# Kernel optimization log

Measured on AMD Instinct MI355X. Metric: run time of the kernel, lower is better.

Reference implementation:

```python
import jax, jax.numpy as jnp
import numpy as np

N, E, D, L, G = 50000, 640000, 128, 5, 128
BN_EPS = 1e-5

def _bn(x, g, b):
    # training-mode batchnorm over axis 0, biased variance (torch semantics)
    m = x.mean(axis=0)
    v = x.var(axis=0)
    return (x - m) * jax.lax.rsqrt(v + BN_EPS) * g + b

def setup_inputs():
    key = jax.random.key(0)
    ks = iter(jax.random.split(key, 40))
    rn = lambda shape, s=0.05: jax.random.normal(next(ks), shape, jnp.float32) * s
    inp = {}
    inp['x'] = jax.random.randint(next(ks), (N, 1), 0, 300)
    inp['edge_index'] = jax.random.randint(next(ks), (2, E), 0, N)
    inp['edge_attr'] = jax.random.normal(next(ks), (E, 7), jnp.float32)
    inp['batch'] = jnp.sort(jax.random.randint(next(ks), (N,), 0, G))
    inp['node_emb'] = rn((300, D))
    inp['vn_emb'] = jnp.zeros((1, D), jnp.float32)
    inp['eps'] = jnp.zeros((L,), jnp.float32)
    inp['edge_W'] = rn((L, 7, D)); inp['edge_b'] = rn((L, D))
    inp['W1'] = rn((L, D, 2 * D)); inp['b1'] = rn((L, 2 * D))
    inp['bn1_g'] = 1.0 + rn((L, 2 * D)); inp['bn1_b'] = rn((L, 2 * D))
    inp['W2'] = rn((L, 2 * D, D)); inp['b2'] = rn((L, D))
    inp['bn_g'] = 1.0 + rn((L, D)); inp['bn_b'] = rn((L, D))
    inp['vn_W1'] = rn((L - 1, D, 2 * D)); inp['vn_b1'] = rn((L - 1, 2 * D))
    inp['vn_bn1_g'] = 1.0 + rn((L - 1, 2 * D)); inp['vn_bn1_b'] = rn((L - 1, 2 * D))
    inp['vn_W2'] = rn((L - 1, 2 * D, D)); inp['vn_b2'] = rn((L - 1, D))
    inp['vn_bn2_g'] = 1.0 + rn((L - 1, D)); inp['vn_bn2_b'] = rn((L - 1, D))
    return inp

def reference(x, edge_index, edge_attr, batch, node_emb, vn_emb, eps,
              edge_W, edge_b, W1, b1, bn1_g, bn1_b, W2, b2, bn_g, bn_b,
              vn_W1, vn_b1, vn_bn1_g, vn_bn1_b, vn_W2, vn_b2, vn_bn2_g, vn_bn2_b):
    src, dst = edge_index[0], edge_index[1]
    h = node_emb[x[:, 0]]                      # [N, D]
    vn = jnp.broadcast_to(vn_emb, (G, D))      # virtualnode state per graph
    for l in range(L):
        h_in = h + vn[batch]                   # virtualnode broadcast
        e = edge_attr @ edge_W[l] + edge_b[l]  # [E, D]
        msg = jax.nn.relu(h_in[src] + e)       # gather + fused elementwise
        agg = jax.ops.segment_sum(msg, dst, num_segments=N)
        z = (1.0 + eps[l]) * h_in + agg
        z = jax.nn.relu(_bn(z @ W1[l] + b1[l], bn1_g[l], bn1_b[l]))
        z = _bn(z @ W2[l] + b2[l], bn_g[l], bn_b[l])
        h_out = jax.nn.relu(z) if l != L - 1 else z
        if l < L - 1:
            pooled = jax.ops.segment_sum(h_in, batch, num_segments=G)
            v = vn + pooled
            v = jax.nn.relu(_bn(v @ vn_W1[l] + vn_b1[l], vn_bn1_g[l], vn_bn1_b[l]))
            vn = jax.nn.relu(_bn(v @ vn_W2[l] + vn_b2[l], vn_bn2_g[l], vn_bn2_b[l]))
        h = h_out
    return h
```

## Files before the change

kernel.cpp:

```cpp
#include <hip/hip_runtime.h>
#include <stdint.h>

#define NN 50000
#define EE 640000
#define DD 128
#define LL 5
#define GG 128
#define D2 256

using bf16x8 = __attribute__((ext_vector_type(8))) short;
using f32x4v = __attribute__((ext_vector_type(4))) float;
using u32x4v = __attribute__((ext_vector_type(4))) unsigned int;

__device__ __forceinline__ unsigned short f2bf(float f){
  union { float f; uint32_t u; } c; c.f = f;
  uint32_t u = c.u;
  uint32_t r = (u + 0x7FFFu + ((u >> 16) & 1u)) >> 16;
  return (unsigned short)r;
}
__device__ __forceinline__ float bf2f(unsigned short u){
  union { uint32_t u; float f; } c; c.u = ((uint32_t)u) << 16; return c.f;
}


__global__ __launch_bounds__(256) void zero_kernel(float* p, int n){
  int i = blockIdx.x*256 + threadIdx.x;
  if (i < n) p[i] = 0.f;
}

__global__ __launch_bounds__(256) void count_kernel(const int* __restrict__ ei, int* __restrict__ counts){
  int e = blockIdx.x*256 + threadIdx.x;
  if (e < EE) atomicAdd(&counts[ei[EE + e]], 1);
}

#define SCAN_B 512
__global__ __launch_bounds__(SCAN_B) void scan1_kernel(const int* __restrict__ counts, int* __restrict__ bsums, int n){
  __shared__ int sh[SCAN_B];
  int b = blockIdx.x, t = threadIdx.x;
  int i = b*SCAN_B + t;
  sh[t] = (i < n) ? counts[i] : 0;
  __syncthreads();
  for (int s = SCAN_B/2; s > 0; s >>= 1){
    if (t < s) sh[t] += sh[t+s];
    __syncthreads();
  }
  if (t == 0) bsums[b] = sh[0];
}

__global__ void scan2_kernel(int* bsums, int nb){
  if (threadIdx.x == 0){
    int run = 0;
    for (int i = 0; i < nb; ++i){ int v = bsums[i]; bsums[i] = run; run += v; }
  }
}

__global__ __launch_bounds__(SCAN_B) void scan3_kernel(const int* __restrict__ counts, const int* __restrict__ bsums,
                                                       int* __restrict__ startp, int* __restrict__ cursor, int n){
  __shared__ int sh[SCAN_B];
  int b = blockIdx.x, t = threadIdx.x;
  int i = b*SCAN_B + t;
  int v = (i < n) ? counts[i] : 0;
  sh[t] = v;
  __syncthreads();
  for (int s = 1; s < SCAN_B; s <<= 1){
    int add = (t >= s) ? sh[t-s] : 0;
    __syncthreads();
    sh[t] += add;
    __syncthreads();
  }
  int excl = sh[t] - v + bsums[b];
  if (i < n){ startp[i] = excl; cursor[i] = excl; }
  if (i == n-1) startp[n] = excl + v;
}

__global__ __launch_bounds__(256) void fill_kernel(const int* __restrict__ ei, int* __restrict__ cursor, int* __restrict__ csr){
  int e = blockIdx.x*256 + threadIdx.x;
  if (e < EE){
    int d = ei[EE + e];
    int slot = atomicAdd(&cursor[d], 1);
    csr[slot] = e;
  }
}

__global__ __launch_bounds__(256) void egather_kernel(const int* __restrict__ csr, const int* __restrict__ ei,
                                                      const float* __restrict__ ea,
                                                      int* __restrict__ csr_src, float* __restrict__ csr_ea8){
  int s = blockIdx.x*256 + threadIdx.x;
  if (s < EE){
    int e = csr[s];
    csr_src[s] = ei[e];
    float v[8];
    #pragma unroll
    for (int k = 0; k < 7; ++k) v[k] = ea[(size_t)e*7 + k];
    v[7] = 0.f;
    #pragma unroll
    for (int k = 0; k < 8; ++k) csr_ea8[(size_t)s*8 + k] = v[k];
  }
}

__global__ __launch_bounds__(256) void wtrans_kernel(const float* __restrict__ W1, const float* __restrict__ W2,
                                                     unsigned short* __restrict__ W1T, unsigned short* __restrict__ W2T){
  int idx = blockIdx.x*256 + threadIdx.x;
  const int total = LL*DD*D2;
  if (idx < total){
    int l = idx / (DD*D2);
    int rem = idx - l*(DD*D2);
    int k = rem / D2;
    int c = rem - k*D2;
    W1T[(size_t)l*32768 + (size_t)c*128 + k] = f2bf(W1[idx]);
  } else if (idx < 2*total){
    int j = idx - total;
    int l = j / (DD*D2);
    int rem = j - l*(DD*D2);
    int k = rem / DD;
    int c = rem - k*DD;
    W2T[(size_t)l*32768 + (size_t)c*256 + k] = f2bf(W2[j]);
  }
}

__global__ __launch_bounds__(128) void init_kernel(const int* __restrict__ x, const int* __restrict__ batch,
                                                   const float* __restrict__ emb, const float* __restrict__ vn_emb,
                                                   unsigned short* __restrict__ hin_bf, float* __restrict__ vbuf0,
                                                   float* __restrict__ vn){
  int r0 = blockIdx.x*128;
  int r1 = r0 + 128; if (r1 > NN) r1 = NN;
  int d = threadIdx.x;
  float ve = vn_emb[d];
  if (blockIdx.x == 0){
    for (int g = 0; g < GG; ++g) vn[(size_t)g*DD + d] = ve;
  }
  __shared__ int sb[128];
  __shared__ int sx[128];
  if (r0 + d < r1){ sb[d] = batch[r0 + d]; sx[d] = x[r0 + d]; }
  __syncthreads();
  int curg = sb[0];
  float pacc = 0.f;
  for (int r = r0; r < r1; ++r){
    int g = sb[r - r0];
    if (g != curg){
      atomicAdd(&vbuf0[(size_t)curg*DD + d], pacc);
      pacc = 0.f; curg = g;
    }
    float hv = emb[(size_t)sx[r - r0]*DD + d] + ve;
    hin_bf[(size_t)r*DD + d] = f2bf(hv);
    pacc += hv;
  }
  atomicAdd(&vbuf0[(size_t)curg*DD + d], pacc);
}


__global__ __launch_bounds__(128) void agg2_kernel(const unsigned short* __restrict__ hin_bf,
                                                   const int* __restrict__ csr_src, const float* __restrict__ csr_ea8,
                                                   const int* __restrict__ startp,
                                                   const float* __restrict__ eW, const float* __restrict__ eb,
                                                   const float* __restrict__ eps, int l,
                                                   unsigned short* __restrict__ zout){
  int node = blockIdx.x, d = threadIdx.x;
  int s0 = startp[node], s1 = startp[node+1];
  float w[7];
  #pragma unroll
  for (int k = 0; k < 7; ++k) w[k] = eW[k*128 + d];
  float bd = eb[d];
  float acc = 0.f;
  __shared__ int ssrc[32];
  __shared__ float sattr[32][8];
  for (int base = s0; base < s1; base += 32){
    int cnt = min(32, s1 - base);
    __syncthreads();
    if (d < cnt) ssrc[d] = csr_src[base + d];
    for (int q = d; q < cnt*8; q += 128){
      sattr[q >> 3][q & 7] = csr_ea8[(size_t)base*8 + q];
    }
    __syncthreads();
    for (int j = 0; j < cnt; ++j){
      float hv = bf2f(hin_bf[(size_t)ssrc[j]*128 + d]);
      float e = bd;
      #pragma unroll
      for (int k = 0; k < 7; ++k) e += sattr[j][k]*w[k];
      float m = hv + e;
      acc += (m > 0.f) ? m : 0.f;
    }
  }
  float one = 1.f + eps[l];
  float z = one*bf2f(hin_bf[(size_t)node*128 + d]) + acc;
  zout[(size_t)node*128 + d] = f2bf(z);
}

__global__ __launch_bounds__(256) void gemm1_kernel(const unsigned short* __restrict__ A,
                                                    const unsigned short* __restrict__ BT,
                                                    const float* __restrict__ bias,
                                                    unsigned short* __restrict__ Y,
                                                    float* __restrict__ sums, float* __restrict__ sqs){
  __shared__ __align__(16) unsigned short Al[128*128];
  __shared__ __align__(16) unsigned short Bl[128*128];
  const int t = threadIdx.x;
  const int rb = blockIdx.x, cb = blockIdx.y;
  for (int it = 0; it < 8; ++it){
    int idx = it*256 + t;
    int row = idx >> 4, ch = idx & 15;
    int grow = rb*128 + row;
    u32x4v v = {0,0,0,0};
    if (grow < NN) v = *(const u32x4v*)(A + (size_t)grow*128 + ch*8);
    *(u32x4v*)((char*)Al + row*256 + ((ch*16) ^ ((row&7)<<4))) = v;
  }
  for (int it = 0; it < 8; ++it){
    int idx = it*256 + t;
    int row = idx >> 4, ch = idx & 15;
    u32x4v v = *(const u32x4v*)(BT + (size_t)(cb*128 + row)*128 + ch*8);
    *(u32x4v*)((char*)Bl + row*256 + ((ch*16) ^ ((row&7)<<4))) = v;
  }
  __syncthreads();
  const int lane = t & 63, wave = t >> 6;
  const int wm = wave >> 1, wn = wave & 1;
  const int r0 = lane & 15, kg = lane >> 4;
  f32x4v acc[4][4] = {};
  #pragma unroll
  for (int kk = 0; kk < 4; ++kk){
    const int kb = kk*64 + kg*16;
    bf16x8 a[4], b[4];
    #pragma unroll
    for (int m = 0; m < 4; ++m){
      int row = wm*64 + m*16 + r0;
      a[m] = *(const bf16x8*)((const char*)Al + row*256 + (kb ^ ((r0&7)<<4)));
    }
    #pragma unroll
    for (int n = 0; n < 4; ++n){
      int col = wn*64 + n*16 + r0;
      b[n] = *(const bf16x8*)((const char*)Bl + col*256 + (kb ^ ((r0&7)<<4)));
    }
    #pragma unroll
    for (int m = 0; m < 4; ++m)
      #pragma unroll
      for (int n = 0; n < 4; ++n)
        acc[m][n] = __builtin_amdgcn_mfma_f32_16x16x32_bf16(a[m], b[n], acc[m][n], 0, 0, 0);
  }
  #pragma unroll
  for (int n = 0; n < 4; ++n){
    const int col = cb*128 + wn*64 + n*16 + r0;
    const float bv = bias[col];
    float s = 0.f, q = 0.f;
    #pragma unroll
    for (int m = 0; m < 4; ++m){
      const int rowb = rb*128 + wm*64 + m*16 + kg*4;
      #pragma unroll
      for (int j = 0; j < 4; ++j){
        int grow = rowb + j;
        if (grow < NN){
          float v = acc[m][n][j] + bv;
          Y[(size_t)grow*256 + col] = f2bf(v);
          s += v; q += v*v;
        }
      }
    }
    s += __shfl_xor(s, 16); q += __shfl_xor(q, 16);
    s += __shfl_xor(s, 32); q += __shfl_xor(q, 32);
    if (kg == 0){ atomicAdd(&sums[col], s); atomicAdd(&sqs[col], q); }
  }
}

template<int FINAL>
__global__ __launch_bounds__(256) void gemm2_kernel(const unsigned short* __restrict__ Yin,
                                                    const float* __restrict__ sum1, const float* __restrict__ sq1,
                                                    const float* __restrict__ bg, const float* __restrict__ bb,
                                                    const unsigned short* __restrict__ BT,
                                                    const float* __restrict__ bias,
                                                    unsigned short* __restrict__ Yh, float* __restrict__ Yf,
                                                    float* __restrict__ sums, float* __restrict__ sqs){
  __shared__ __align__(16) unsigned short Al[128*128];
  __shared__ __align__(16) unsigned short Bl[128*128];
  __shared__ float s_scl[256], s_shf[256];
  const int t = threadIdx.x;
  const int rb = blockIdx.x;
  {
    const float invn = 1.f/(float)NN;
    float m = sum1[t]*invn;
    float var = sq1[t]*invn - m*m;
    var = var > 0.f ? var : 0.f;
    float sc = bg[t]*rsqrtf(var + 1e-5f);
    s_scl[t] = sc;
    s_shf[t] = bb[t] - m*sc;
  }
  const int lane = t & 63, wave = t >> 6;
  const int wm = wave >> 1, wn = wave & 1;
  const int r0 = lane & 15, kg = lane >> 4;
  f32x4v acc[4][4] = {};
  for (int kt = 0; kt < 2; ++kt){
    __syncthreads();
    for (int it = 0; it < 8; ++it){
      int idx = it*256 + t;
      int row = idx >> 4, ch = idx & 15;
      int grow = rb*128 + row;
      int c0 = kt*128 + ch*8;
      u32x4v pv = {0,0,0,0};
      if (grow < NN){
        u32x4v yv = *(const u32x4v*)(Yin + (size_t)grow*256 + c0);
        unsigned short tb[8];
        #pragma unroll
        for (int jj = 0; jj < 4; ++jj){
          uint32_t pw = yv[jj];
          float a0 = bf2f((unsigned short)(pw & 0xFFFFu));
          float a1 = bf2f((unsigned short)(pw >> 16));
          float v0 = a0*s_scl[c0 + 2*jj]     + s_shf[c0 + 2*jj];
          float v1 = a1*s_scl[c0 + 2*jj + 1] + s_shf[c0 + 2*jj + 1];
          tb[2*jj]     = f2bf(v0 > 0.f ? v0 : 0.f);
          tb[2*jj + 1] = f2bf(v1 > 0.f ? v1 : 0.f);
        }
        pv[0] = (uint32_t)tb[0] | ((uint32_t)tb[1] << 16);
        pv[1] = (uint32_t)tb[2] | ((uint32_t)tb[3] << 16);
        pv[2] = (uint32_t)tb[4] | ((uint32_t)tb[5] << 16);
        pv[3] = (uint32_t)tb[6] | ((uint32_t)tb[7] << 16);
      }
      *(u32x4v*)((char*)Al + row*256 + ((ch*16) ^ ((row&7)<<4))) = pv;
    }
    for (int it = 0; it < 8; ++it){
      int idx = it*256 + t;
      int row = idx >> 4, ch = idx & 15;
      u32x4v v = *(const u32x4v*)(BT + (size_t)row*256 + kt*128 + ch*8);
      *(u32x4v*)((char*)Bl + row*256 + ((ch*16) ^ ((row&7)<<4))) = v;
    }
    __syncthreads();
    #pragma unroll
    for (int kk = 0; kk < 4; ++kk){
      const int kb = kk*64 + kg*16;
      bf16x8 a[4], b[4];
      #pragma unroll
      for (int m = 0; m < 4; ++m){
        int row = wm*64 + m*16 + r0;
        a[m] = *(const bf16x8*)((const char*)Al + row*256 + (kb ^ ((r0&7)<<4)));
      }
      #pragma unroll
      for (int n = 0; n < 4; ++n){
        int col = wn*64 + n*16 + r0;
        b[n] = *(const bf16x8*)((const char*)Bl + col*256 + (kb ^ ((r0&7)<<4)));
      }
      #pragma unroll
      for (int m = 0; m < 4; ++m)
        #pragma unroll
        for (int n = 0; n < 4; ++n)
          acc[m][n] = __builtin_amdgcn_mfma_f32_16x16x32_bf16(a[m], b[n], acc[m][n], 0, 0, 0);
    }
  }
  #pragma unroll
  for (int n = 0; n < 4; ++n){
    const int col = wn*64 + n*16 + r0;
    const float bv = bias[col];
    float s = 0.f, q = 0.f;
    #pragma unroll
    for (int m = 0; m < 4; ++m){
      const int rowb = rb*128 + wm*64 + m*16 + kg*4;
      #pragma unroll
      for (int j = 0; j < 4; ++j){
        int grow = rowb + j;
        if (grow < NN){
          float v = acc[m][n][j] + bv;
          if (FINAL) Yf[(size_t)grow*128 + col] = v;
          else       Yh[(size_t)grow*128 + col] = f2bf(v);
          s += v; q += v*v;
        }
      }
    }
    s += __shfl_xor(s, 16); q += __shfl_xor(q, 16);
    s += __shfl_xor(s, 32); q += __shfl_xor(q, 32);
    if (kg == 0){ atomicAdd(&sums[col], s); atomicAdd(&sqs[col], q); }
  }
}

__global__ __launch_bounds__(128) void happly_fused_kernel(const unsigned short* __restrict__ y2h,
                                                           const float* __restrict__ sum2, const float* __restrict__ sq2,
                                                           const float* __restrict__ bg, const float* __restrict__ bb,
                                                           const float* __restrict__ vn, const int* __restrict__ batch,
                                                           unsigned short* __restrict__ hin_bf, float* __restrict__ vbuf_next){
  int r0 = blockIdx.x*128;
  int r1 = r0 + 128; if (r1 > NN) r1 = NN;
  int d = threadIdx.x;
  const float invn = 1.f/(float)NN;
  float m = sum2[d]*invn;
  float var = sq2[d]*invn - m*m;
  var = var > 0.f ? var : 0.f;
  float sc = bg[d]*rsqrtf(var + 1e-5f);
  float sh = bb[d] - m*sc;
  __shared__ int sb[128];
  if (r0 + d < r1) sb[d] = batch[r0 + d];
  __syncthreads();
  int curg = sb[0];
  float vnv = vn[(size_t)curg*DD + d];
  float pacc = 0.f;
  for (int r = r0; r < r1; ++r){
    int g = sb[r - r0];
    if (g != curg){
      atomicAdd(&vbuf_next[(size_t)curg*DD + d], pacc);
      pacc = 0.f; curg = g;
      vnv = vn[(size_t)curg*DD + d];
    }
    float y = bf2f(y2h[(size_t)r*DD + d]);
    float v = y*sc + sh;
    v = v > 0.f ? v : 0.f;
    float hv = v + vnv;
    hin_bf[(size_t)r*DD + d] = f2bf(hv);
    pacc += hv;
  }
  atomicAdd(&vbuf_next[(size_t)curg*DD + d], pacc);
}

__global__ __launch_bounds__(256) void happly_final_kernel(float* __restrict__ y,
                                                           const float* __restrict__ sum2, const float* __restrict__ sq2,
                                                           const float* __restrict__ bg, const float* __restrict__ bb){
  int idx = blockIdx.x*256 + threadIdx.x;
  if (idx >= NN*32) return;
  int c4 = idx & 31;
  const float invn = 1.f/(float)NN;
  f32x4v yv = *(const f32x4v*)(y + (size_t)idx*4);
  f32x4v o;
  #pragma unroll
  for (int j = 0; j < 4; ++j){
    int c = c4*4 + j;
    float m = sum2[c]*invn;
    float var = sq2[c]*invn - m*m;
    var = var > 0.f ? var : 0.f;
    float sc = bg[c]*rsqrtf(var + 1e-5f);
    o[j] = (yv[j] - m)*sc + bb[c];
  }
  *(f32x4v*)(y + (size_t)idx*4) = o;
}

__global__ __launch_bounds__(256) void vmlp1_kernel(const float* __restrict__ vn, const float* __restrict__ vbufl,
                                                    const float* __restrict__ W, const float* __restrict__ bias,
                                                    float* __restrict__ Yo,
                                                    float* __restrict__ sums, float* __restrict__ sqs){
  __shared__ float vrow[128];
  int r = blockIdx.x, c = threadIdx.x;
  if (c < 128) vrow[c] = vn[r*128 + c] + vbufl[r*128 + c];
  __syncthreads();
  float acc = 0.f;
  #pragma unroll 8
  for (int k = 0; k < 128; ++k) acc += vrow[k]*W[k*256 + c];
  float y = acc + bias[c];
  Yo[r*256 + c] = y;
  atomicAdd(&sums[c], y);
  atomicAdd(&sqs[c], y*y);
}

__global__ __launch_bounds__(128) void vmlp2_kernel(const float* __restrict__ Yin,
                                                    const float* __restrict__ sumv1, const float* __restrict__ sqv1,
                                                    const float* __restrict__ vg, const float* __restrict__ vb,
                                                    const float* __restrict__ W, const float* __restrict__ bias,
                                                    float* __restrict__ Yo,
                                                    float* __restrict__ sums, float* __restrict__ sqs){
  __shared__ float arow[256];
  __shared__ float s_scl[256], s_shf[256];
  int r = blockIdx.x, c = threadIdx.x;
  const float invg = 1.f/(float)GG;
  for (int k = c; k < 256; k += 128){
    float m = sumv1[k]*invg;
    float var = sqv1[k]*invg - m*m;
    var = var > 0.f ? var : 0.f;
    float sc = vg[k]*rsqrtf(var + 1e-5f);
    s_scl[k] = sc;
    s_shf[k] = vb[k] - m*sc;
  }
  __syncthreads();
  for (int k = c; k < 256; k += 128){
    float a = Yin[r*256 + k]*s_scl[k] + s_shf[k];
    arow[k] = a > 0.f ? a : 0.f;
  }
  __syncthreads();
  float acc = 0.f;
  #pragma unroll 8
  for (int k = 0; k < 256; ++k) acc += arow[k]*W[k*128 + c];
  float y = acc + bias[c];
  Yo[r*128 + c] = y;
  atomicAdd(&sums[c], y);
  atomicAdd(&sqs[c], y*y);
}

__global__ __launch_bounds__(256) void va_kernel(const float* __restrict__ yv2,
                                                 const float* __restrict__ sumv2, const float* __restrict__ sqv2,
                                                 const float* __restrict__ vg, const float* __restrict__ vb,
                                                 float* __restrict__ vn){
  int idx = blockIdx.x*256 + threadIdx.x;
  if (idx < GG*128){
    int c = idx & 127;
    const float invg = 1.f/(float)GG;
    float m = sumv2[c]*invg;
    float var = sqv2[c]*invg - m*m;
    var = var > 0.f ? var : 0.f;
    float sc = vg[c]*rsqrtf(var + 1e-5f);
    float v = (yv2[idx] - m)*sc + vb[c];
    vn[idx] = v > 0.f ? v : 0.f;
  }
}


extern "C" void kernel_launch(void* const* d_in, const int* in_sizes, int n_in,
                              void* d_out, int out_size, void* d_ws, size_t ws_size,
                              hipStream_t stream){
  const int*   x         = (const int*)  d_in[0];
  const int*   ei        = (const int*)  d_in[1];
  const float* edge_attr = (const float*)d_in[2];
  const int*   batch     = (const int*)  d_in[3];
  const float* node_emb  = (const float*)d_in[4];
  const float* vn_emb    = (const float*)d_in[5];
  const float* eps       = (const float*)d_in[6];
  const float* edge_W    = (const float*)d_in[7];
  const float* edge_b    = (const float*)d_in[8];
  const float* W1        = (const float*)d_in[9];
  const float* b1        = (const float*)d_in[10];
  const float* bn1_g     = (const float*)d_in[11];
  const float* bn1_b     = (const float*)d_in[12];
  const float* W2        = (const float*)d_in[13];
  const float* b2        = (const float*)d_in[14];
  const float* bn_g      = (const float*)d_in[15];
  const float* bn_b      = (const float*)d_in[16];
  const float* vn_W1     = (const float*)d_in[17];
  const float* vn_b1     = (const float*)d_in[18];
  const float* vn_bn1_g  = (const float*)d_in[19];
  const float* vn_bn1_b  = (const float*)d_in[20];
  const float* vn_W2     = (const float*)d_in[21];
  const float* vn_b2     = (const float*)d_in[22];
  const float* vn_bn2_g  = (const float*)d_in[23];
  const float* vn_bn2_b  = (const float*)d_in[24];
  float* hout = (float*)d_out;

  char* ws = (char*)d_ws;
  size_t off = 0;
  auto alloc = [&](size_t bytes)->char*{
    char* p = ws + off; off += (bytes + 255) & ~(size_t)255; return p;
  };
  unsigned short* hin_bf = (unsigned short*)alloc((size_t)NN*DD*2);
  unsigned short* zy     = (unsigned short*)alloc((size_t)NN*DD*2);
  unsigned short* y1h    = (unsigned short*)alloc((size_t)NN*D2*2);
  float*          vn     = (float*)         alloc((size_t)GG*DD*4);
  float*          yv1    = (float*)         alloc((size_t)GG*D2*4);
  float*          yv2    = (float*)         alloc((size_t)GG*DD*4);
  unsigned short* W1T    = (unsigned short*)alloc((size_t)LL*D2*DD*2);
  unsigned short* W2T    = (unsigned short*)alloc((size_t)LL*D2*DD*2);
  const int STATS_F = LL*8*256;
  const int VBUF_F  = 5*GG*DD;
  const int ZTOT    = STATS_F + VBUF_F + NN;
  float* zeroreg = (float*)alloc((size_t)ZTOT*4);
  float* stats_all = zeroreg;
  float* vbuf_all  = zeroreg + STATS_F;
  int*   counts    = (int*)(zeroreg + STATS_F + VBUF_F);
  int*   startp = (int*)  alloc((size_t)(NN+1)*4);
  int*   cursor = (int*)  alloc((size_t)NN*4);
  int*   csr    = (int*)  alloc((size_t)EE*4);
  int*   bsums  = (int*)  alloc(128*4);
  int*   csr_src= (int*)  alloc((size_t)EE*4);
  float* csr_ea8= (float*)alloc((size_t)EE*8*4);

  const int nb_scan = (NN + SCAN_B - 1)/SCAN_B;
  const int row_blocks = (NN + 127)/128;
  const int ew_blocks = (NN*32 + 255)/256;

  zero_kernel<<<(ZTOT + 255)/256, 256, 0, stream>>>(zeroreg, ZTOT);
  count_kernel<<<EE/256, 256, 0, stream>>>(ei, counts);
  scan1_kernel<<<nb_scan, SCAN_B, 0, stream>>>(counts, bsums, NN);
  scan2_kernel<<<1, 64, 0, stream>>>(bsums, nb_scan);
  scan3_kernel<<<nb_scan, SCAN_B, 0, stream>>>(counts, bsums, startp, cursor, NN);
  fill_kernel<<<EE/256, 256, 0, stream>>>(ei, cursor, csr);
  egather_kernel<<<EE/256, 256, 0, stream>>>(csr, ei, edge_attr, csr_src, csr_ea8);
  wtrans_kernel<<<(2*LL*DD*D2 + 255)/256, 256, 0, stream>>>(W1, W2, W1T, W2T);
  init_kernel<<<row_blocks, 128, 0, stream>>>(x, batch, node_emb, vn_emb, hin_bf, vbuf_all, vn);

  for (int l = 0; l < LL; ++l){
    float* st    = stats_all + (size_t)l*8*256;
    float* sum1  = st + 0*256, *sq1  = st + 1*256;
    float* sum2  = st + 2*256, *sq2  = st + 3*256;
    float* sumv1 = st + 4*256, *sqv1 = st + 5*256;
    float* sumv2 = st + 6*256, *sqv2 = st + 7*256;

    agg2_kernel<<<NN, 128, 0, stream>>>(hin_bf, csr_src, csr_ea8, startp,
                                        edge_W + (size_t)l*7*DD, edge_b + (size_t)l*DD, eps, l, zy);
    gemm1_kernel<<<dim3(row_blocks, 2), 256, 0, stream>>>(zy, W1T + (size_t)l*32768,
                                                          b1 + (size_t)l*D2, y1h, sum1, sq1);
    if (l != LL-1){
      gemm2_kernel<0><<<row_blocks, 256, 0, stream>>>(y1h, sum1, sq1,
                                                      bn1_g + (size_t)l*D2, bn1_b + (size_t)l*D2,
                                                      W2T + (size_t)l*32768, b2 + (size_t)l*DD,
                                                      zy, nullptr, sum2, sq2);
      float* vbufl = vbuf_all + (size_t)l*GG*DD;
      float* vbufn = vbuf_all + (size_t)(l+1)*GG*DD;
      vmlp1_kernel<<<GG, 256, 0, stream>>>(vn, vbufl, vn_W1 + (size_t)l*DD*D2, vn_b1 + (size_t)l*D2,
                                           yv1, sumv1, sqv1);
      vmlp2_kernel<<<GG, 128, 0, stream>>>(yv1, sumv1, sqv1,
                                           vn_bn1_g + (size_t)l*D2, vn_bn1_b + (size_t)l*D2,
                                           vn_W2 + (size_t)l*D2*DD, vn_b2 + (size_t)l*DD,
                                           yv2, sumv2, sqv2);
      va_kernel<<<(GG*DD + 255)/256, 256, 0, stream>>>(yv2, sumv2, sqv2,
                                                       vn_bn2_g + (size_t)l*DD, vn_bn2_b + (size_t)l*DD, vn);
      happly_fused_kernel<<<row_blocks, 128, 0, stream>>>(zy, sum2, sq2,
                                                          bn_g + (size_t)l*DD, bn_b + (size_t)l*DD,
                                                          vn, batch, hin_bf, vbufn);
    } else {
      gemm2_kernel<1><<<row_blocks, 256, 0, stream>>>(y1h, sum1, sq1,
                                                      bn1_g + (size_t)l*D2, bn1_b + (size_t)l*D2,
                                                      W2T + (size_t)l*32768, b2 + (size_t)l*DD,
                                                      nullptr, hout, sum2, sq2);
      happly_final_kernel<<<ew_blocks, 256, 0, stream>>>(hout, sum2, sq2,
                                                         bn_g + (size_t)l*DD, bn_b + (size_t)l*DD);
    }
  }
  (void)in_sizes; (void)n_in; (void)out_size; (void)ws_size;
}
```

Measured before the change: 1.263 ms.

## Aggregate one node per wavefront with two features per lane

The edge-aggregation kernel now assigns one node to each 64-lane wavefront, packing four nodes into a 256-thread block. Each lane handles two adjacent features through 32-bit bf16-pair loads. Edge indices and attributes are read directly from global memory with vector loads instead of being staged in shared memory, which removes the per-chunk __syncthreads barriers. The cost is redundant per-lane loads of edge attributes, served from cache, and possible wave imbalance when node degrees vary.

```diff
diff --git a/kernel.cpp b/kernel.cpp
--- a/kernel.cpp
+++ b/kernel.cpp
@@ -20,6 +20,12 @@
 }
 __device__ __forceinline__ float bf2f(unsigned short u){
   union { uint32_t u; float f; } c; c.u = ((uint32_t)u) << 16; return c.f;
+}
+__device__ __forceinline__ float bf2f_lo(uint32_t p){
+  union { uint32_t u; float f; } c; c.u = p << 16; return c.f;
+}
+__device__ __forceinline__ float bf2f_hi(uint32_t p){
+  union { uint32_t u; float f; } c; c.u = p & 0xFFFF0000u; return c.f;
 }
 
 
@@ -149,41 +155,47 @@
 }
 
 
-__global__ __launch_bounds__(128) void agg2_kernel(const unsigned short* __restrict__ hin_bf,
+__global__ __launch_bounds__(256) void agg3_kernel(const unsigned short* __restrict__ hin_bf,
                                                    const int* __restrict__ csr_src, const float* __restrict__ csr_ea8,
                                                    const int* __restrict__ startp,
                                                    const float* __restrict__ eW, const float* __restrict__ eb,
                                                    const float* __restrict__ eps, int l,
                                                    unsigned short* __restrict__ zout){
-  int node = blockIdx.x, d = threadIdx.x;
-  int s0 = startp[node], s1 = startp[node+1];
-  float w[7];
+  const int wid  = threadIdx.x >> 6;
+  const int lane = threadIdx.x & 63;
+  const int node = blockIdx.x*4 + wid;
+  const int s0 = startp[node], s1 = startp[node+1];
+  float2 w[7];
   #pragma unroll
-  for (int k = 0; k < 7; ++k) w[k] = eW[k*128 + d];
-  float bd = eb[d];
-  float acc = 0.f;
-  __shared__ int ssrc[32];
-  __shared__ float sattr[32][8];
-  for (int base = s0; base < s1; base += 32){
-    int cnt = min(32, s1 - base);
-    __syncthreads();
-    if (d < cnt) ssrc[d] = csr_src[base + d];
-    for (int q = d; q < cnt*8; q += 128){
-      sattr[q >> 3][q & 7] = csr_ea8[(size_t)base*8 + q];
-    }
-    __syncthreads();
-    for (int j = 0; j < cnt; ++j){
-      float hv = bf2f(hin_bf[(size_t)ssrc[j]*128 + d]);
-      float e = bd;
-      #pragma unroll
-      for (int k = 0; k < 7; ++k) e += sattr[j][k]*w[k];
-      float m = hv + e;
-      acc += (m > 0.f) ? m : 0.f;
-    }
-  }
-  float one = 1.f + eps[l];
-  float z = one*bf2f(hin_bf[(size_t)node*128 + d]) + acc;
-  zout[(size_t)node*128 + d] = f2bf(z);
+  for (int k = 0; k < 7; ++k) w[k] = *(const float2*)(eW + k*128 + lane*2);
+  const float2 bd = *(const float2*)(eb + lane*2);
+  float acc0 = 0.f, acc1 = 0.f;
+  #pragma unroll 2
+  for (int s = s0; s < s1; ++s){
+    int src = csr_src[s];
+    f32x4v a0 = *(const f32x4v*)(csr_ea8 + (size_t)s*8);
+    f32x4v a1 = *(const f32x4v*)(csr_ea8 + (size_t)s*8 + 4);
+    uint32_t h2 = *(const uint32_t*)(hin_bf + (size_t)src*128 + lane*2);
+    float h0 = bf2f_lo(h2), h1 = bf2f_hi(h2);
+    float e0 = bd.x, e1 = bd.y;
+    e0 += a0[0]*w[0].x; e1 += a0[0]*w[0].y;
+    e0 += a0[1]*w[1].x; e1 += a0[1]*w[1].y;
+    e0 += a0[2]*w[2].x; e1 += a0[2]*w[2].y;
+    e0 += a0[3]*w[3].x; e1 += a0[3]*w[3].y;
+    e0 += a1[0]*w[4].x; e1 += a1[0]*w[4].y;
+    e0 += a1[1]*w[5].x; e1 += a1[1]*w[5].y;
+    e0 += a1[2]*w[6].x; e1 += a1[2]*w[6].y;
+    float m0 = h0 + e0;
+    float m1 = h1 + e1;
+    acc0 += (m0 > 0.f) ? m0 : 0.f;
+    acc1 += (m1 > 0.f) ? m1 : 0.f;
+  }
+  const float one = 1.f + eps[l];
+  uint32_t hs = *(const uint32_t*)(hin_bf + (size_t)node*128 + lane*2);
+  float z0 = one*bf2f_lo(hs) + acc0;
+  float z1 = one*bf2f_hi(hs) + acc1;
+  uint32_t out = (uint32_t)f2bf(z0) | ((uint32_t)f2bf(z1) << 16);
+  *(uint32_t*)(zout + (size_t)node*128 + lane*2) = out;
 }
 
 __global__ __launch_bounds__(256) void gemm1_kernel(const unsigned short* __restrict__ A,
@@ -569,8 +581,8 @@
     float* sumv1 = st + 4*256, *sqv1 = st + 5*256;
     float* sumv2 = st + 6*256, *sqv2 = st + 7*256;
 
-    agg2_kernel<<<NN, 128, 0, stream>>>(hin_bf, csr_src, csr_ea8, startp,
-                                        edge_W + (size_t)l*7*DD, edge_b + (size_t)l*DD, eps, l, zy);
+    agg3_kernel<<<NN/4, 256, 0, stream>>>(hin_bf, csr_src, csr_ea8, startp,
+                                          edge_W + (size_t)l*7*DD, edge_b + (size_t)l*DD, eps, l, zy);
     gemm1_kernel<<<dim3(row_blocks, 2), 256, 0, stream>>>(zy, W1T + (size_t)l*32768,
                                                           b1 + (size_t)l*D2, y1h, sum1, sq1);
     if (l != LL-1){
```

New measurement: 1.295 ms. 2.6% more time.
